# Optimization experiments

Measured on AMD Instinct MI355X. Metric: run time of the kernel, lower is better.

## Reference

```python
import jax, jax.numpy as jnp
import numpy as np

B, N = 256, 100000

def setup_inputs() -> dict:
    key = jax.random.key(0)
    k1, k2 = jax.random.split(key)
    preds = jax.random.normal(k1, (B, N), dtype=jnp.float32)
    labels = jax.random.normal(k2, (B, N), dtype=jnp.float32)
    return {"preds": preds, "labels": labels, "subject": 0}

def reference(preds, labels, subject):
    # Batch-parallel Pearson: five fused row reductions instead of a Python loop.
    n = jnp.asarray(preds.shape[1], preds.dtype)
    sum_x = jnp.sum(preds, axis=1)
    sum_y = jnp.sum(labels, axis=1)
    sum_xy = jnp.sum(preds * labels, axis=1)
    sum_x2 = jnp.sum(preds * preds, axis=1)
    sum_y2 = jnp.sum(labels * labels, axis=1)
    num = n * sum_xy - sum_x * sum_y
    den = jnp.sqrt((n * sum_x2 - sum_x ** 2) * (n * sum_y2 - sum_y ** 2))
    pearson = num / den
    return jnp.mean(1.0 - pearson)
```

## Files before the change

kernel.cpp:

```cpp
#include <hip/hip_runtime.h>

#define B_ROWS   256
#define SPLIT    8
#define NTHREADS 256

__global__ __launch_bounds__(NTHREADS) void pearson_partial(
    const float* __restrict__ preds,
    const float* __restrict__ labels,
    float* __restrict__ ws,
    int N)
{
    const int row = blockIdx.x / SPLIT;
    const int seg = blockIdx.x % SPLIT;
    const int tid = threadIdx.x;

    const int n4      = N / 4;
    const int per_seg = n4 / SPLIT;
    const int begin   = seg * per_seg;
    const int end     = begin + per_seg;

    const float4* p4 = reinterpret_cast<const float4*>(preds  + (size_t)row * N);
    const float4* l4 = reinterpret_cast<const float4*>(labels + (size_t)row * N);

    float sx = 0.f, sy = 0.f, sxy = 0.f, sxx = 0.f, syy = 0.f;

    for (int i = begin + tid; i < end; i += NTHREADS) {
        float4 a = p4[i];
        float4 b = l4[i];
        sx += a.x; sy += b.x; sxy = fmaf(a.x, b.x, sxy); sxx = fmaf(a.x, a.x, sxx); syy = fmaf(b.x, b.x, syy);
        sx += a.y; sy += b.y; sxy = fmaf(a.y, b.y, sxy); sxx = fmaf(a.y, a.y, sxx); syy = fmaf(b.y, b.y, syy);
        sx += a.z; sy += b.z; sxy = fmaf(a.z, b.z, sxy); sxx = fmaf(a.z, a.z, sxx); syy = fmaf(b.z, b.z, syy);
        sx += a.w; sy += b.w; sxy = fmaf(a.w, b.w, sxy); sxx = fmaf(a.w, a.w, sxx); syy = fmaf(b.w, b.w, syy);
    }

    for (int o = 32; o > 0; o >>= 1) {
        sx  += __shfl_down(sx,  o, 64);
        sy  += __shfl_down(sy,  o, 64);
        sxy += __shfl_down(sxy, o, 64);
        sxx += __shfl_down(sxx, o, 64);
        syy += __shfl_down(syy, o, 64);
    }

    __shared__ float red[4][5];
    const int wave = tid >> 6;
    const int lane = tid & 63;
    if (lane == 0) {
        red[wave][0] = sx;  red[wave][1] = sy;  red[wave][2] = sxy;
        red[wave][3] = sxx; red[wave][4] = syy;
    }
    __syncthreads();

    if (tid == 0) {
        float t0 = red[0][0] + red[1][0] + red[2][0] + red[3][0];
        float t1 = red[0][1] + red[1][1] + red[2][1] + red[3][1];
        float t2 = red[0][2] + red[1][2] + red[2][2] + red[3][2];
        float t3 = red[0][3] + red[1][3] + red[2][3] + red[3][3];
        float t4 = red[0][4] + red[1][4] + red[2][4] + red[3][4];
        float* w = ws + (size_t)blockIdx.x * 5;
        w[0] = t0; w[1] = t1; w[2] = t2; w[3] = t3; w[4] = t4;
    }
}

__global__ __launch_bounds__(NTHREADS) void pearson_final(
    const float* __restrict__ ws,
    float* __restrict__ out,
    int N)
{
    const int t = threadIdx.x;

    double sx = 0.0, sy = 0.0, sxy = 0.0, sxx = 0.0, syy = 0.0;
    for (int s = 0; s < SPLIT; ++s) {
        const float* w = ws + ((size_t)t * SPLIT + s) * 5;
        sx  += (double)w[0];
        sy  += (double)w[1];
        sxy += (double)w[2];
        sxx += (double)w[3];
        syy += (double)w[4];
    }

    const double n   = (double)N;
    const double num = n * sxy - sx * sy;
    const double den = sqrt((n * sxx - sx * sx) * (n * syy - sy * sy));
    double val = 1.0 - num / den;

    for (int o = 32; o > 0; o >>= 1)
        val += __shfl_down(val, o, 64);

    __shared__ double red[4];
    const int wave = t >> 6;
    const int lane = t & 63;
    if (lane == 0) red[wave] = val;
    __syncthreads();

    if (t == 0) {
        double total = red[0] + red[1] + red[2] + red[3];
        out[0] = (float)(total / (double)B_ROWS);
    }
}

extern "C" void kernel_launch(void* const* d_in, const int* in_sizes, int n_in,
                              void* d_out, int out_size, void* d_ws, size_t ws_size,
                              hipStream_t stream)
{
    const float* preds  = (const float*)d_in[0];
    const float* labels = (const float*)d_in[1];

    const int N = in_sizes[0] / B_ROWS;

    float* ws  = (float*)d_ws;
    float* out = (float*)d_out;

    pearson_partial<<<B_ROWS * SPLIT, NTHREADS, 0, stream>>>(preds, labels, ws, N);
    pearson_final<<<1, NTHREADS, 0, stream>>>(ws, out, N);
}
```

Before: 37.60 us.

## Fuse final Pearson reduction into partial kernel via last-block ticket

Merges the two kernels into one. Each block writes its partial sums, then increments an atomic ticket, and the last block to finish performs the cross-segment reduction and writes the output. This removes the second kernel launch but adds a memset of the ticket before the launch. The main loop is also restructured into a counted, unrolled loop with a remainder tail, and the launch bounds now include an occupancy hint.

```diff
diff --git a/kernel.cpp b/kernel.cpp
--- a/kernel.cpp
+++ b/kernel.cpp
@@ -3,28 +3,46 @@
 #define B_ROWS   256
 #define SPLIT    8
 #define NTHREADS 256
+#define NBLOCKS  (B_ROWS * SPLIT)
 
-__global__ __launch_bounds__(NTHREADS) void pearson_partial(
+#define TICKET_OFF (NBLOCKS * 5 * sizeof(float))
+
+__global__ __launch_bounds__(NTHREADS, 8) void pearson_fused(
     const float* __restrict__ preds,
     const float* __restrict__ labels,
     float* __restrict__ ws,
+    unsigned int* __restrict__ ticket,
+    float* __restrict__ out,
     int N)
 {
-    const int row = blockIdx.x / SPLIT;
-    const int seg = blockIdx.x % SPLIT;
+    const int bid = blockIdx.x;
+    const int row = bid >> 3;
+    const int seg = bid & (SPLIT - 1);
     const int tid = threadIdx.x;
 
-    const int n4      = N / 4;
+    const int n4      = N >> 2;
     const int per_seg = n4 / SPLIT;
     const int begin   = seg * per_seg;
-    const int end     = begin + per_seg;
 
     const float4* p4 = reinterpret_cast<const float4*>(preds  + (size_t)row * N);
     const float4* l4 = reinterpret_cast<const float4*>(labels + (size_t)row * N);
 
     float sx = 0.f, sy = 0.f, sxy = 0.f, sxx = 0.f, syy = 0.f;
 
-    for (int i = begin + tid; i < end; i += NTHREADS) {
+    const int full = per_seg / NTHREADS;
+    const int rem  = per_seg - full * NTHREADS;
+
+    int i = begin + tid;
+#pragma unroll 4
+    for (int k = 0; k < full; ++k, i += NTHREADS) {
+        float4 a = p4[i];
+        float4 b = l4[i];
+        sx += a.x; sy += b.x; sxy = fmaf(a.x, b.x, sxy); sxx = fmaf(a.x, a.x, sxx); syy = fmaf(b.x, b.x, syy);
+        sx += a.y; sy += b.y; sxy = fmaf(a.y, b.y, sxy); sxx = fmaf(a.y, a.y, sxx); syy = fmaf(b.y, b.y, syy);
+        sx += a.z; sy += b.z; sxy = fmaf(a.z, b.z, sxy); sxx = fmaf(a.z, a.z, sxx); syy = fmaf(b.z, b.z, syy);
+        sx += a.w; sy += b.w; sxy = fmaf(a.w, b.w, sxy); sxx = fmaf(a.w, a.w, sxx); syy = fmaf(b.w, b.w, syy);
+    }
+    if (tid < rem) {
         float4 a = p4[i];
         float4 b = l4[i];
         sx += a.x; sy += b.x; sxy = fmaf(a.x, b.x, sxy); sxx = fmaf(a.x, a.x, sxx); syy = fmaf(b.x, b.x, syy);
@@ -42,6 +60,7 @@
     }
 
     __shared__ float red[4][5];
+    __shared__ int   s_last;
     const int wave = tid >> 6;
     const int lane = tid & 63;
     if (lane == 0) {
@@ -51,51 +70,47 @@
     __syncthreads();
 
     if (tid == 0) {
-        float t0 = red[0][0] + red[1][0] + red[2][0] + red[3][0];
-        float t1 = red[0][1] + red[1][1] + red[2][1] + red[3][1];
-        float t2 = red[0][2] + red[1][2] + red[2][2] + red[3][2];
-        float t3 = red[0][3] + red[1][3] + red[2][3] + red[3][3];
-        float t4 = red[0][4] + red[1][4] + red[2][4] + red[3][4];
-        float* w = ws + (size_t)blockIdx.x * 5;
-        w[0] = t0; w[1] = t1; w[2] = t2; w[3] = t3; w[4] = t4;
+        float* w = ws + (size_t)bid * 5;
+        w[0] = red[0][0] + red[1][0] + red[2][0] + red[3][0];
+        w[1] = red[0][1] + red[1][1] + red[2][1] + red[3][1];
+        w[2] = red[0][2] + red[1][2] + red[2][2] + red[3][2];
+        w[3] = red[0][3] + red[1][3] + red[2][3] + red[3][3];
+        w[4] = red[0][4] + red[1][4] + red[2][4] + red[3][4];
+        __threadfence();
+        unsigned int old = atomicAdd(ticket, 1u);
+        s_last = (old == NBLOCKS - 1) ? 1 : 0;
     }
-}
+    __syncthreads();
+    if (!s_last) return;
 
-__global__ __launch_bounds__(NTHREADS) void pearson_final(
-    const float* __restrict__ ws,
-    float* __restrict__ out,
-    int N)
-{
-    const int t = threadIdx.x;
+    __threadfence();
 
-    double sx = 0.0, sy = 0.0, sxy = 0.0, sxx = 0.0, syy = 0.0;
+    const int t = tid;
+    double dsx = 0.0, dsy = 0.0, dsxy = 0.0, dsxx = 0.0, dsyy = 0.0;
+#pragma unroll
     for (int s = 0; s < SPLIT; ++s) {
         const float* w = ws + ((size_t)t * SPLIT + s) * 5;
-        sx  += (double)w[0];
-        sy  += (double)w[1];
-        sxy += (double)w[2];
-        sxx += (double)w[3];
-        syy += (double)w[4];
+        dsx  += (double)w[0];
+        dsy  += (double)w[1];
+        dsxy += (double)w[2];
+        dsxx += (double)w[3];
+        dsyy += (double)w[4];
     }
 
     const double n   = (double)N;
-    const double num = n * sxy - sx * sy;
-    const double den = sqrt((n * sxx - sx * sx) * (n * syy - sy * sy));
+    const double num = n * dsxy - dsx * dsy;
+    const double den = sqrt((n * dsxx - dsx * dsx) * (n * dsyy - dsy * dsy));
     double val = 1.0 - num / den;
 
     for (int o = 32; o > 0; o >>= 1)
         val += __shfl_down(val, o, 64);
 
-    __shared__ double red[4];
-    const int wave = t >> 6;
-    const int lane = t & 63;
-    if (lane == 0) red[wave] = val;
+    __shared__ double dred[4];
+    if (lane == 0) dred[wave] = val;
     __syncthreads();
 
-    if (t == 0) {
-        double total = red[0] + red[1] + red[2] + red[3];
-        out[0] = (float)(total / (double)B_ROWS);
-    }
+    if (tid == 0)
+        out[0] = (float)((dred[0] + dred[1] + dred[2] + dred[3]) / (double)B_ROWS);
 }
 
 extern "C" void kernel_launch(void* const* d_in, const int* in_sizes, int n_in,
@@ -107,9 +122,10 @@
 
     const int N = in_sizes[0] / B_ROWS;
 
-    float* ws  = (float*)d_ws;
-    float* out = (float*)d_out;
+    float*        ws     = (float*)d_ws;
+    unsigned int* ticket = (unsigned int*)((char*)d_ws + TICKET_OFF);
+    float*        out    = (float*)d_out;
 
-    pearson_partial<<<B_ROWS * SPLIT, NTHREADS, 0, stream>>>(preds, labels, ws, N);
-    pearson_final<<<1, NTHREADS, 0, stream>>>(ws, out, N);
+    hipMemsetAsync(ticket, 0, sizeof(unsigned int), stream);
+    pearson_fused<<<NBLOCKS, NTHREADS, 0, stream>>>(preds, labels, ws, ticket, out, N);
 }
```

Result: slower. 103.6 us (+175.6%).
